# Optimization experiments

Measured on AMD Instinct MI355X. Metric: run time of the kernel, lower is better.

Reference implementation:

```python
import jax, jax.numpy as jnp
import numpy as np

DIM = 1024
NUM_HEADS = 16
HEAD_DIM = DIM // NUM_HEADS
SCALE = HEAD_DIM ** -0.5
B, N = 4, 2048


def setup_inputs() -> dict:
    key = jax.random.key(0)
    ks = jax.random.split(key, 5)
    s = 1.0 / np.sqrt(DIM)  # ~ torch Linear init scale
    x = jax.random.normal(ks[0], (B, N, DIM), dtype=jnp.float32)
    Wq = jax.random.normal(ks[1], (DIM, DIM), dtype=jnp.float32) * s
    Wk = jax.random.normal(ks[2], (DIM, DIM), dtype=jnp.float32) * s
    Wv = jax.random.normal(ks[3], (DIM, DIM), dtype=jnp.float32) * s
    Wo = jax.random.normal(ks[4], (DIM, DIM), dtype=jnp.float32) * s
    mask = jnp.tril(jnp.ones((N, N), dtype=bool))  # causal 2D bool mask
    return {"x": x, "mask": mask, "Wq": Wq, "Wk": Wk, "Wv": Wv, "Wo": Wo}


def reference(x, mask, Wq, Wk, Wv, Wo):
    Bb, Nn, D = x.shape
    def split_heads(t):
        return t.reshape(Bb, Nn, NUM_HEADS, HEAD_DIM).transpose(0, 2, 1, 3)  # [B,H,N,d]
    q = split_heads(x @ Wq.T)
    k = split_heads(x @ Wk.T)
    v = split_heads(x @ Wv.T)
    attn = jnp.einsum('bhqd,bhkd->bhqk', q, k) * SCALE  # [B,H,N,N]
    # 2D mask -> broadcast over batch and heads; ~mask positions set to -inf
    attn = jnp.where(mask[None, None, :, :], attn, -jnp.inf)
    attn = jax.nn.softmax(attn, axis=-1)
    out = jnp.einsum('bhqk,bhkd->bhqd', attn, v)
    out = out.transpose(0, 2, 1, 3).reshape(Bb, Nn, D)
    return out @ Wo.T
```

## Files before the change

### kernel.cpp

```cpp
#include <hip/hip_runtime.h>
#include <stdint.h>

#define Bq   4
#define Nseq 2048
#define NH   16
#define HD   64
#define DIMD 1024

typedef float  f32x4   __attribute__((ext_vector_type(4)));
typedef float  f32x16  __attribute__((ext_vector_type(16)));
typedef __bf16 bf16x8  __attribute__((ext_vector_type(8)));
typedef short  s16x4   __attribute__((ext_vector_type(4)));

typedef __attribute__((address_space(1))) void as1_void;
typedef __attribute__((address_space(3))) void as3_void;

static __device__ __forceinline__ uint16_t f2bf(float f) {
    uint32_t u = __builtin_bit_cast(uint32_t, f);
    u += 0x7fffu + ((u >> 16) & 1u);
    return (uint16_t)(u >> 16);
}

static __device__ __forceinline__ uint32_t pk2(float a, float b) {
    uint32_t ua = __builtin_bit_cast(uint32_t, a);
    uint32_t ub = __builtin_bit_cast(uint32_t, b);
    return (ua >> 16) | (ub & 0xffff0000u);
}

static __device__ __forceinline__ void asyncLoad16(const uint16_t* g, uint16_t* l) {
    __builtin_amdgcn_global_load_lds((as1_void*)g, (as3_void*)l, 16, 0, 0);
}

static __device__ __forceinline__ void storeOut(float* p, float v)    { *p = v; }
static __device__ __forceinline__ void storeOut(uint16_t* p, float v) { *p = f2bf(v); }

__global__ void cast_all(const float* __restrict__ x,
                         const float* __restrict__ wq, const float* __restrict__ wk,
                         const float* __restrict__ wv, const float* __restrict__ wo,
                         uint16_t* __restrict__ dst) {
    size_t i = ((size_t)blockIdx.x * blockDim.x + threadIdx.x) * 4;
    const float* src; size_t off; float scale = 1.0f;
    if (i < 8388608) { src = x; off = i; }
    else {
        size_t wI = i - 8388608;
        size_t wi = wI >> 20;
        off = wI & 1048575;
        src = (wi == 0) ? wq : (wi == 1) ? wk : (wi == 2) ? wv : wo;
        if (wi == 0) scale = 0.18033688011112042f;
    }
    float4 v = *(const float4*)(src + off);
    ushort4 o;
    o.x = f2bf(v.x * scale); o.y = f2bf(v.y * scale);
    o.z = f2bf(v.z * scale); o.w = f2bf(v.w * scale);
    *(ushort4*)(dst + i) = o;
}

__global__ __launch_bounds__(512, 2) void gemm_qkv384(
    const uint16_t* __restrict__ A, const uint16_t* __restrict__ W0,
    uint16_t* __restrict__ C0, uint16_t* __restrict__ vtb)
{
    __shared__ __align__(16) uint16_t Asm[2][2][4096];
    __shared__ __align__(16) uint16_t Bsm[2][2][12288];

    const int t = threadIdx.x, lane = t & 63, w = t >> 6;
    const int wm = w >> 2, wn = w & 3;
    const int ln = lane & 15, l4 = lane >> 4;

    const int m0 = blockIdx.x * 128;
    const int n0 = blockIdx.y * 384;

    const int srow = t >> 3;
    const int sg   = (t & 7) ^ (srow & 7);
    const uint16_t* aBase = A + (size_t)(m0 + (srow >> 5)*64 + (srow & 31))*DIMD + sg*8;
    const uint16_t* bBase[3];
    #pragma unroll
    for (int j = 0; j < 3; ++j) {
        int f = j*64 + srow;
        int wnf = f / 48, off = f % 48;
        bBase[j] = W0 + (size_t)(n0 + wnf*96 + off)*DIMD + sg*8;
    }

#define SA(mh_, buf_, kk_) asyncLoad16(aBase + (size_t)(mh_)*32*DIMD + (kk_), \
        &Asm[buf_][mh_][t*8])
#define SB(nh_, j_, buf_, kk_) asyncLoad16(bBase[j_] + (size_t)(nh_)*48*DIMD + (kk_), \
        &Bsm[buf_][nh_][(j_)*4096 + t*8])

    SA(0,0,0); SA(1,0,0);
    SB(0,0,0,0); SB(0,1,0,0); SB(0,2,0,0);
    SB(1,0,0,0); SB(1,1,0,0); SB(1,2,0,0);
    SA(0,1,64);
    SB(0,0,1,64); SB(0,1,1,64); SB(0,2,1,64);
    asm volatile("s_waitcnt vmcnt(4)" ::: "memory");
    __builtin_amdgcn_s_barrier();

    const int cs0 = ( l4      ^ (ln & 7)) * 8;
    const int cs1 = ((4 + l4) ^ (ln & 7)) * 8;
    const int awo = wm*2048 + ln*64;
    const int bwo = wn*3072 + ln*64;

    bf16x8 af[2][2], bf0[3][2], bf1[3][2];
    f32x4 acc[4][6] = {};

#define LDA(mh_, buf_)                                                         \
    _Pragma("unroll")                                                          \
    for (int mf = 0; mf < 2; ++mf) {                                           \
        af[mf][0] = *(const bf16x8*)(&Asm[buf_][mh_][awo + mf*1024 + cs0]);    \
        af[mf][1] = *(const bf16x8*)(&Asm[buf_][mh_][awo + mf*1024 + cs1]);    \
    }
#define LDB(nh_, buf_, BF)                                                     \
    _Pragma("unroll")                                                          \
    for (int nf = 0; nf < 3; ++nf) {                                           \
        BF[nf][0] = *(const bf16x8*)(&Bsm[buf_][nh_][bwo + nf*1024 + cs0]);    \
        BF[nf][1] = *(const bf16x8*)(&Bsm[buf_][nh_][bwo + nf*1024 + cs1]);    \
    }
#define MFMA12(mh_, nh_, BF)                                                   \
    _Pragma("unroll")                                                          \
    for (int mf = 0; mf < 2; ++mf)                                             \
        _Pragma("unroll")                                                      \
        for (int nf = 0; nf < 3; ++nf) {                                       \
            acc[(mh_)*2+mf][(nh_)*3+nf] = __builtin_amdgcn_mfma_f32_16x16x32_bf16( \
                af[mf][0], BF[nf][0], acc[(mh_)*2+mf][(nh_)*3+nf], 0,0,0);     \
            acc[(mh_)*2+mf][(nh_)*3+nf] = __builtin_amdgcn_mfma_f32_16x16x32_bf16( \
                af[mf][1], BF[nf][1], acc[(mh_)*2+mf][(nh_)*3+nf], 0,0,0);     \
        }
#define BARR()  __builtin_amdgcn_s_barrier()
#define SCB0()  __builtin_amdgcn_sched_barrier(0)
#define LGKM()  asm volatile("s_waitcnt lgkmcnt(0)" ::: "memory")
#define PRIO1() __builtin_amdgcn_s_setprio(1)
#define PRIO0() __builtin_amdgcn_s_setprio(0)

    #pragma unroll 1
    for (int i = 0; i < 8; ++i) {
        const int kk1 = i*128 + 64, kk2 = i*128 + 128, kk3 = i*128 + 192;
        const bool pf = (i < 7);

        LDA(0,0); LDB(0,0,bf0);
        SA(1,1,kk1); SB(1,0,1,kk1);
        BARR(); LGKM(); SCB0();
        PRIO1(); MFMA12(0,0,bf0); PRIO0();
        SCB0(); BARR();

        LDB(1,0,bf1);
        SB(1,1,1,kk1); SB(1,2,1,kk1);
        BARR(); LGKM(); SCB0();
        PRIO1(); MFMA12(0,1,bf1); PRIO0();
        SCB0(); BARR();

        LDA(1,0);
        if (pf) { SA(0,0,kk2); SB(0,0,0,kk2); }
        BARR(); LGKM(); SCB0();
        PRIO1(); MFMA12(1,0,bf0); PRIO0();
        SCB0(); BARR();

        if (pf) { SB(0,1,0,kk2); SB(0,2,0,kk2); }
        BARR(); SCB0();
        PRIO1(); MFMA12(1,1,bf1); PRIO0();
        SCB0();
        if (pf) { asm volatile("s_waitcnt vmcnt(4)" ::: "memory"); }
        else    { asm volatile("s_waitcnt vmcnt(0)" ::: "memory"); }
        BARR();

        LDA(0,1); LDB(0,1,bf0);
        if (pf) { SA(1,0,kk2); SB(1,0,0,kk2); }
        BARR(); LGKM(); SCB0();
        PRIO1(); MFMA12(0,0,bf0); PRIO0();
        SCB0(); BARR();

        LDB(1,1,bf1);
        if (pf) { SB(1,1,0,kk2); SB(1,2,0,kk2); }
        BARR(); LGKM(); SCB0();
        PRIO1(); MFMA12(0,1,bf1); PRIO0();
        SCB0(); BARR();

        LDA(1,1);
        if (pf) { SA(0,1,kk3); SB(0,0,1,kk3); }
        BARR(); LGKM(); SCB0();
        PRIO1(); MFMA12(1,0,bf0); PRIO0();
        SCB0(); BARR();

        if (pf) { SB(0,1,1,kk3); SB(0,2,1,kk3); }
        BARR(); SCB0();
        PRIO1(); MFMA12(1,1,bf1); PRIO0();
        SCB0();
        if (pf) { asm volatile("s_waitcnt vmcnt(4)" ::: "memory"); BARR(); }
    }

#undef SA
#undef SB
#undef LDA
#undef LDB
#undef MFMA12

    #pragma unroll
    for (int mh = 0; mh < 2; ++mh)
      #pragma unroll
      for (int mf = 0; mf < 2; ++mf)
        #pragma unroll
        for (int nh = 0; nh < 2; ++nh)
          #pragma unroll
          for (int nf = 0; nf < 3; ++nf) {
              const f32x4 a4 = acc[mh*2+mf][nh*3+nf];
              int rowg = m0 + wm*64 + mh*32 + mf*16 + l4*4;
              int colg = n0 + wn*96 + nh*48 + nf*16 + ln;
              if (colg < 2048) {
                  uint16_t* C = C0 + (size_t)(colg >> 10) * 8388608;
                  int col = colg & 1023;
                  #pragma unroll
                  for (int r = 0; r < 4; ++r)
                      C[(size_t)(rowg + r)*1024 + col] = f2bf(a4[r]);
              } else {
                  int dg = colg - 2048;
                  int bb = rowg >> 11, nn = rowg & 2047;
                  ushort4 o4;
                  o4.x = f2bf(a4[0]); o4.y = f2bf(a4[1]);
                  o4.z = f2bf(a4[2]); o4.w = f2bf(a4[3]);
                  *(ushort4*)(vtb + ((size_t)(bb*1024 + dg))*Nseq + nn) = o4;
              }
          }
}

template <typename OutT>
__global__ __launch_bounds__(256) void gemm_bt(
    const uint16_t* __restrict__ A, const uint16_t* __restrict__ W0,
    OutT* __restrict__ C0, int K, int Nld, int blocksPerSec,
    size_t wSecStride, size_t cSecStride, uint16_t* __restrict__ vtb, int vSec)
{
    __shared__ __align__(16) uint16_t As[128*64];
    __shared__ __align__(16) uint16_t Bs[128*64];

    const int t = threadIdx.x, lane = t & 63, w = t >> 6;
    const int wr = w >> 1, wc = w & 1;
    const int half = lane >> 5, ml = lane & 31;

    const int m0  = blockIdx.x * 128;
    const int sec = blockIdx.y / blocksPerSec;
    const int n0  = (blockIdx.y % blocksPerSec) * 128;
    const uint16_t* Wp = W0 + (size_t)sec * wSecStride;
    OutT* C = C0 + (size_t)sec * cSecStride;

    int srow[4], sg[4];
    #pragma unroll
    for (int i = 0; i < 4; ++i) {
        int s = t + 256*i;
        srow[i] = s >> 3;
        sg[i]   = (s & 7) ^ (srow[i] & 7);
    }

    int arow[2], brow[2];
    #pragma unroll
    for (int i = 0; i < 2; ++i) {
        arow[i] = wr*64 + i*32 + ml;
        brow[i] = wc*64 + i*32 + ml;
    }

    f32x16 acc[2][2] = {};

    for (int k0 = 0; k0 < K; k0 += 64) {
        __syncthreads();
        #pragma unroll
        for (int i = 0; i < 4; ++i) {
            asyncLoad16(A  + (size_t)(m0 + srow[i])*K + k0 + sg[i]*8,
                        As + (size_t)(w*64 + 256*i)*8);
            asyncLoad16(Wp + (size_t)(n0 + srow[i])*K + k0 + sg[i]*8,
                        Bs + (size_t)(w*64 + 256*i)*8);
        }
        __syncthreads();

        #pragma unroll
        for (int s = 0; s < 4; ++s) {
            const int chunk = s*2 + half;
            bf16x8 af[2], bfr[2];
            #pragma unroll
            for (int i = 0; i < 2; ++i) {
                int m = arow[i];
                af[i]  = *(const bf16x8*)(As + (size_t)(m*8 + (chunk ^ (m & 7)))*8);
                int n = brow[i];
                bfr[i] = *(const bf16x8*)(Bs + (size_t)(n*8 + (chunk ^ (n & 7)))*8);
            }
            #pragma unroll
            for (int mt = 0; mt < 2; ++mt)
                #pragma unroll
                for (int nt = 0; nt < 2; ++nt)
                    acc[mt][nt] = __builtin_amdgcn_mfma_f32_32x32x16_bf16(
                        af[mt], bfr[nt], acc[mt][nt], 0, 0, 0);
        }
    }

    if (vtb != nullptr && sec == vSec) {
        #pragma unroll
        for (int mt = 0; mt < 2; ++mt)
            #pragma unroll
            for (int nt = 0; nt < 2; ++nt) {
                int colg = n0 + wc*64 + nt*32 + ml;
                int hh = colg >> 6, dd = colg & 63;
                #pragma unroll
                for (int g = 0; g < 4; ++g) {
                    int rowg = m0 + wr*64 + mt*32 + 8*g + 4*half;
                    int bb = rowg >> 11, nn = rowg & 2047;
                    ushort4 o4;
                    o4.x = f2bf(acc[mt][nt][4*g + 0]);
                    o4.y = f2bf(acc[mt][nt][4*g + 1]);
                    o4.z = f2bf(acc[mt][nt][4*g + 2]);
                    o4.w = f2bf(acc[mt][nt][4*g + 3]);
                    *(ushort4*)(vtb + ((size_t)((bb*NH + hh)*HD + dd))*Nseq + nn) = o4;
                }
            }
    } else {
        #pragma unroll
        for (int mt = 0; mt < 2; ++mt)
            #pragma unroll
            for (int nt = 0; nt < 2; ++nt) {
                int col = n0 + wc*64 + nt*32 + ml;
                #pragma unroll
                for (int r = 0; r < 16; ++r) {
                    int row = m0 + wr*64 + mt*32 + (r & 3) + 8*(r >> 2) + 4*half;
                    storeOut(&C[(size_t)row * Nld + col], acc[mt][nt][r]);
                }
            }
    }
}

__global__ __launch_bounds__(256, 3) void attn(
    const uint16_t* __restrict__ Q, const uint16_t* __restrict__ K,
    const uint16_t* __restrict__ Vt, uint16_t* __restrict__ O)
{
    __shared__ __align__(16) uint16_t Kb[3][64*64];
    __shared__ __align__(16) uint16_t Vb[3][64*64];

    const int t = threadIdx.x, lane = t & 63, w = t >> 6;
    const int quad = lane >> 4, c = lane & 15;
    const int y = blockIdx.y;
    const int qi = (y < 4) ? (15 - y) : (y < 8) ? (y + 4) : (y < 12) ? (y - 4) : (15 - y);
    const int q0 = qi * 128;
    const int bh = blockIdx.x, b = bh >> 4, h = bh & 15;
    const size_t tokBase = (size_t)b * Nseq;
    const int hcol = h * HD;
    uint16_t* Qs = (uint16_t*)Kb;

    #define STAGE_KV(k0_, buf_)                                             \
        _Pragma("unroll")                                                    \
        for (int i = 0; i < 2; ++i) {                                        \
            int s = t + 256*i;                                               \
            int row = s >> 3, gg = (s & 7) ^ (row & 7);                      \
            asyncLoad16(K + (tokBase + (k0_) + row)*DIMD + hcol + gg*8,      \
                        Kb[buf_] + (size_t)(w*64 + 256*i)*8);                \
            asyncLoad16(Vt + ((size_t)bh*HD + row)*Nseq + (k0_) + gg*8,      \
                        Vb[buf_] + (size_t)(w*64 + 256*i)*8);                \
        }

    #pragma unroll
    for (int i = 0; i < 4; ++i) {
        int s = t + 256*i;
        int row = s >> 3, gg = (s & 7) ^ (row & 7);
        asyncLoad16(Q + (tokBase + q0 + row)*DIMD + hcol + gg*8,
                    Qs + (size_t)(w*64 + 256*i)*8);
    }
    __syncthreads();
    bf16x8 qf[2][2];
    #pragma unroll
    for (int qt = 0; qt < 2; ++qt)
        #pragma unroll
        for (int ks = 0; ks < 2; ++ks) {
            int row = w*32 + qt*16 + c;
            int pos = (ks*4 + quad) ^ (row & 7);
            qf[qt][ks] = *(const bf16x8*)(Qs + (size_t)(row*8 + pos)*8);
        }
    __syncthreads();

    const int wrow0 = q0 + w*32;
    const int end = 2*qi + 2;
    STAGE_KV(0, 0);
    STAGE_KV(64, 1);

    f32x4  o[2][4] = {};
    float  l_lane[2] = {0.f, 0.f};
    int b0 = 0, b1 = 1, b2 = 2;

    for (int kt = 0; kt < end; ++kt) {
        const int k0 = kt * 64;

        if (kt + 1 < end) { asm volatile("s_waitcnt vmcnt(4)\n\ts_barrier" ::: "memory"); }
        else              { asm volatile("s_waitcnt vmcnt(0)\n\ts_barrier" ::: "memory"); }

        if (kt + 2 < end) { STAGE_KV((kt+2)*64, b2); }

        if (k0 <= wrow0 + 31) {
            const uint16_t* Ks = Kb[b0];
            const uint16_t* Vs = Vb[b0];

            f32x4 sv[2][4] = {};
            __builtin_amdgcn_s_setprio(1);
            #pragma unroll
            for (int nt = 0; nt < 4; ++nt)
                #pragma unroll
                for (int ks = 0; ks < 2; ++ks) {
                    int row = nt*16 + c;
                    int pos = (ks*4 + quad) ^ (row & 7);
                    bf16x8 kf = *(const bf16x8*)(Ks + (size_t)(row*8 + pos)*8);
                    sv[0][nt] = __builtin_amdgcn_mfma_f32_16x16x32_bf16(kf, qf[0][ks], sv[0][nt], 0, 0, 0);
                    sv[1][nt] = __builtin_amdgcn_mfma_f32_16x16x32_bf16(kf, qf[1][ks], sv[1][nt], 0, 0, 0);
                }
            __builtin_amdgcn_s_setprio(0);

            if (k0 + 63 > wrow0) {
                #pragma unroll
                for (int qt = 0; qt < 2; ++qt)
                    #pragma unroll
                    for (int nt = 0; nt < 4; ++nt)
                        #pragma unroll
                        for (int r = 0; r < 4; ++r) {
                            int kvg = k0 + nt*16 + quad*4 + r;
                            int qg  = wrow0 + qt*16 + c;
                            if (kvg > qg) sv[qt][nt][r] = -340.0f;
                        }
            }

            s16x4 pb[2][4];
            #pragma unroll
            for (int qt = 0; qt < 2; ++qt)
                #pragma unroll
                for (int nt = 0; nt < 4; ++nt) {
                    float p0 = __builtin_amdgcn_exp2f(sv[qt][nt][0]);
                    float p1 = __builtin_amdgcn_exp2f(sv[qt][nt][1]);
                    float p2 = __builtin_amdgcn_exp2f(sv[qt][nt][2]);
                    float p3 = __builtin_amdgcn_exp2f(sv[qt][nt][3]);
                    l_lane[qt] += (p0 + p1) + (p2 + p3);
                    union { uint32_t u[2]; s16x4 v; } pu;
                    pu.u[0] = pk2(p0, p1);
                    pu.u[1] = pk2(p2, p3);
                    pb[qt][nt] = pu.v;
                }

            __builtin_amdgcn_s_setprio(1);
            #pragma unroll
            for (int s4 = 0; s4 < 4; ++s4)
                #pragma unroll
                for (int dt = 0; dt < 4; ++dt) {
                    int row = dt*16 + c;
                    int chunk = s4*2 + (quad >> 1);
                    int pos = chunk ^ (row & 7);
                    s16x4 vf = *(const s16x4*)(Vs + (size_t)(row*8 + pos)*8 + (quad & 1)*4);
                    o[0][dt] = __builtin_amdgcn_mfma_f32_16x16x16bf16_1k(vf, pb[0][s4], o[0][dt], 0, 0, 0);
                    o[1][dt] = __builtin_amdgcn_mfma_f32_16x16x16bf16_1k(vf, pb[1][s4], o[1][dt], 0, 0, 0);
                }
            __builtin_amdgcn_s_setprio(0);
        }

        int tmp = b0; b0 = b1; b1 = b2; b2 = tmp;
    }

    #pragma unroll
    for (int qt = 0; qt < 2; ++qt) {
        float l = l_lane[qt];
        l += __shfl_xor(l, 16);
        l += __shfl_xor(l, 32);
        float inv = 1.0f / l;
        int tok = (int)(q0 + w*32 + qt*16 + c);
        #pragma unroll
        for (int dt = 0; dt < 4; ++dt) {
            ushort4 o4;
            o4.x = f2bf(o[qt][dt][0] * inv);
            o4.y = f2bf(o[qt][dt][1] * inv);
            o4.z = f2bf(o[qt][dt][2] * inv);
            o4.w = f2bf(o[qt][dt][3] * inv);
            *(ushort4*)(O + (tokBase + tok)*DIMD + hcol + dt*16 + quad*4) = o4;
        }
    }
    #undef STAGE_KV
}

extern "C" void kernel_launch(void* const* d_in, const int* in_sizes, int n_in,
                              void* d_out, int out_size, void* d_ws, size_t ws_size,
                              hipStream_t stream) {
    const float* x  = (const float*)d_in[0];
    const float* Wq = (const float*)d_in[2];
    const float* Wk = (const float*)d_in[3];
    const float* Wv = (const float*)d_in[4];
    const float* Wo = (const float*)d_in[5];

    uint16_t* ws  = (uint16_t*)d_ws;
    uint16_t* xb  = ws;
    uint16_t* wqb = ws + 8388608;
    uint16_t* wob = wqb + 3*1048576;
    uint16_t* qb  = ws + 12582912;
    uint16_t* kb  = qb + 8388608;
    uint16_t* vtb = kb + 8388608;
    uint16_t* ab  = xb;

    cast_all<<<12288, 256, 0, stream>>>(x, Wq, Wk, Wv, Wo, ws);

    gemm_qkv384<<<dim3(64, 8), 512, 0, stream>>>(xb, wqb, qb, vtb);

    attn<<<dim3(64, 16), 256, 0, stream>>>(qb, kb, vtb, ab);

    gemm_bt<float><<<dim3(64, 8), 256, 0, stream>>>(
        ab, wob, (float*)d_out, DIMD, DIMD, 8, (size_t)0, (size_t)0, nullptr, -1);
}
```

Before: 247.7 us.

## Replace output projection GEMM with pipelined 256x128 double-buffered kernel

The generic gemm_bt used for the output projection is replaced by a dedicated gemm_out256 kernel modeled on the QKV kernel: 512 threads, 256x128 tiles, double-buffered async global-to-LDS loads with phased barriers, priority raising around MFMA blocks, and 16x16x32 MFMAs. It aims to hide load latency behind compute instead of the load-sync-compute loop. The grid shrinks to 256 blocks, which may underfill the 256 CUs with one wave of large blocks, and the store pattern writes fp32 with 16-wide column runs.

```diff
diff --git a/kernel.cpp b/kernel.cpp
--- a/kernel.cpp
+++ b/kernel.cpp
@@ -30,9 +30,6 @@
 static __device__ __forceinline__ void asyncLoad16(const uint16_t* g, uint16_t* l) {
     __builtin_amdgcn_global_load_lds((as1_void*)g, (as3_void*)l, 16, 0, 0);
 }
-
-static __device__ __forceinline__ void storeOut(float* p, float v)    { *p = v; }
-static __device__ __forceinline__ void storeOut(uint16_t* p, float v) { *p = f2bf(v); }
 
 __global__ void cast_all(const float* __restrict__ x,
                          const float* __restrict__ wq, const float* __restrict__ wk,
@@ -55,6 +52,12 @@
     *(ushort4*)(dst + i) = o;
 }
 
+#define BARR()  __builtin_amdgcn_s_barrier()
+#define SCB0()  __builtin_amdgcn_sched_barrier(0)
+#define LGKM()  asm volatile("s_waitcnt lgkmcnt(0)" ::: "memory")
+#define PRIO1() __builtin_amdgcn_s_setprio(1)
+#define PRIO0() __builtin_amdgcn_s_setprio(0)
+
 __global__ __launch_bounds__(512, 2) void gemm_qkv384(
     const uint16_t* __restrict__ A, const uint16_t* __restrict__ W0,
     uint16_t* __restrict__ C0, uint16_t* __restrict__ vtb)
@@ -91,7 +94,7 @@
     SA(0,1,64);
     SB(0,0,1,64); SB(0,1,1,64); SB(0,2,1,64);
     asm volatile("s_waitcnt vmcnt(4)" ::: "memory");
-    __builtin_amdgcn_s_barrier();
+    BARR();
 
     const int cs0 = ( l4      ^ (ln & 7)) * 8;
     const int cs1 = ((4 + l4) ^ (ln & 7)) * 8;
@@ -123,11 +126,6 @@
             acc[(mh_)*2+mf][(nh_)*3+nf] = __builtin_amdgcn_mfma_f32_16x16x32_bf16( \
                 af[mf][1], BF[nf][1], acc[(mh_)*2+mf][(nh_)*3+nf], 0,0,0);     \
         }
-#define BARR()  __builtin_amdgcn_s_barrier()
-#define SCB0()  __builtin_amdgcn_sched_barrier(0)
-#define LGKM()  asm volatile("s_waitcnt lgkmcnt(0)" ::: "memory")
-#define PRIO1() __builtin_amdgcn_s_setprio(1)
-#define PRIO0() __builtin_amdgcn_s_setprio(0)
 
     #pragma unroll 1
     for (int i = 0; i < 8; ++i) {
@@ -219,105 +217,136 @@
           }
 }
 
-template <typename OutT>
-__global__ __launch_bounds__(256) void gemm_bt(
+__global__ __launch_bounds__(512, 2) void gemm_out256(
     const uint16_t* __restrict__ A, const uint16_t* __restrict__ W0,
-    OutT* __restrict__ C0, int K, int Nld, int blocksPerSec,
-    size_t wSecStride, size_t cSecStride, uint16_t* __restrict__ vtb, int vSec)
+    float* __restrict__ C)
 {
-    __shared__ __align__(16) uint16_t As[128*64];
-    __shared__ __align__(16) uint16_t Bs[128*64];
+    __shared__ __align__(16) uint16_t Asm[2][2][8192];
+    __shared__ __align__(16) uint16_t Bsm[2][2][4096];
 
     const int t = threadIdx.x, lane = t & 63, w = t >> 6;
-    const int wr = w >> 1, wc = w & 1;
-    const int half = lane >> 5, ml = lane & 31;
-
-    const int m0  = blockIdx.x * 128;
-    const int sec = blockIdx.y / blocksPerSec;
-    const int n0  = (blockIdx.y % blocksPerSec) * 128;
-    const uint16_t* Wp = W0 + (size_t)sec * wSecStride;
-    OutT* C = C0 + (size_t)sec * cSecStride;
-
-    int srow[4], sg[4];
+    const int wm = w >> 2, wn = w & 3;
+    const int ln = lane & 15, l4 = lane >> 4;
+
+    const int m0 = blockIdx.x * 256;
+    const int n0 = blockIdx.y * 128;
+
+    const int srow = t >> 3;
+    const int sg   = (t & 7) ^ (srow & 7);
+    const uint16_t* aBase = A + (size_t)(m0 + srow)*DIMD + sg*8;
+    const uint16_t* bBase = W0 + (size_t)(n0 + (srow >> 4)*32 + (srow & 15))*DIMD + sg*8;
+
+#define SA(mh_, j_, buf_, kk_) asyncLoad16(aBase + (size_t)((j_)*128 + (mh_)*64)*DIMD + (kk_), \
+        &Asm[buf_][mh_][(j_)*4096 + t*8])
+#define SB(nh_, buf_, kk_) asyncLoad16(bBase + (size_t)(nh_)*16*DIMD + (kk_), \
+        &Bsm[buf_][nh_][t*8])
+
+    SB(0,0,0); SB(1,0,0);
+    SA(0,0,0,0); SA(0,1,0,0);
+    SA(1,0,0,0); SA(1,1,0,0);
+    SB(0,1,64); SB(1,1,64);
+    SA(0,0,1,64); SA(0,1,1,64);
+    asm volatile("s_waitcnt vmcnt(4)" ::: "memory");
+    BARR();
+
+    const int cs0 = ( l4      ^ (ln & 7)) * 8;
+    const int cs1 = ((4 + l4) ^ (ln & 7)) * 8;
+    const int awo = wm*4096 + ln*64;
+    const int bwo = wn*1024 + ln*64;
+
+    bf16x8 af[4][2], bfA[2], bfB[2];
+    f32x4 acc[8][2] = {};
+
+#define LDA(mh_, buf_)                                                         \
+    _Pragma("unroll")                                                          \
+    for (int mf = 0; mf < 4; ++mf) {                                           \
+        af[mf][0] = *(const bf16x8*)(&Asm[buf_][mh_][awo + mf*1024 + cs0]);    \
+        af[mf][1] = *(const bf16x8*)(&Asm[buf_][mh_][awo + mf*1024 + cs1]);    \
+    }
+#define LDB(nh_, buf_, BF)                                                     \
+    BF[0] = *(const bf16x8*)(&Bsm[buf_][nh_][bwo + cs0]);                      \
+    BF[1] = *(const bf16x8*)(&Bsm[buf_][nh_][bwo + cs1]);
+#define MFMA8(mh_, nh_, BF)                                                    \
+    _Pragma("unroll")                                                          \
+    for (int mf = 0; mf < 4; ++mf) {                                           \
+        acc[(mh_)*4+mf][nh_] = __builtin_amdgcn_mfma_f32_16x16x32_bf16(        \
+            af[mf][0], BF[0], acc[(mh_)*4+mf][nh_], 0,0,0);                    \
+        acc[(mh_)*4+mf][nh_] = __builtin_amdgcn_mfma_f32_16x16x32_bf16(        \
+            af[mf][1], BF[1], acc[(mh_)*4+mf][nh_], 0,0,0);                    \
+    }
+
+    #pragma unroll 1
+    for (int i = 0; i < 8; ++i) {
+        const int kk1 = i*128 + 64, kk2 = i*128 + 128, kk3 = i*128 + 192;
+        const bool pf2 = (i < 7);
+        const bool pf3 = (i < 7);
+
+        LDA(0,0); LDB(0,0,bfA);
+        SA(1,0,1,kk1); SA(1,1,1,kk1);
+        BARR(); LGKM(); SCB0();
+        PRIO1(); MFMA8(0,0,bfA); PRIO0();
+        SCB0(); BARR();
+
+        LDB(1,0,bfB);
+        BARR(); LGKM(); SCB0();
+        PRIO1(); MFMA8(0,1,bfB); PRIO0();
+        SCB0(); BARR();
+
+        LDA(1,0);
+        if (pf2) { SB(0,0,kk2); SB(1,0,kk2); SA(0,0,0,kk2); SA(0,1,0,kk2); }
+        BARR(); LGKM(); SCB0();
+        PRIO1(); MFMA8(1,0,bfA); PRIO0();
+        SCB0(); BARR();
+
+        BARR(); SCB0();
+        PRIO1(); MFMA8(1,1,bfB); PRIO0();
+        SCB0();
+        if (pf2) { asm volatile("s_waitcnt vmcnt(4)" ::: "memory"); }
+        else     { asm volatile("s_waitcnt vmcnt(0)" ::: "memory"); }
+        BARR();
+
+        LDA(0,1); LDB(0,1,bfA);
+        if (pf2) { SA(1,0,0,kk2); SA(1,1,0,kk2); }
+        BARR(); LGKM(); SCB0();
+        PRIO1(); MFMA8(0,0,bfA); PRIO0();
+        SCB0(); BARR();
+
+        LDB(1,1,bfB);
+        BARR(); LGKM(); SCB0();
+        PRIO1(); MFMA8(0,1,bfB); PRIO0();
+        SCB0(); BARR();
+
+        LDA(1,1);
+        if (pf3) { SB(0,1,kk3); SB(1,1,kk3); SA(0,0,1,kk3); SA(0,1,1,kk3); }
+        BARR(); LGKM(); SCB0();
+        PRIO1(); MFMA8(1,0,bfA); PRIO0();
+        SCB0(); BARR();
+
+        BARR(); SCB0();
+        PRIO1(); MFMA8(1,1,bfB); PRIO0();
+        SCB0();
+        if (pf3) { asm volatile("s_waitcnt vmcnt(4)" ::: "memory"); BARR(); }
+    }
+
+#undef SA
+#undef SB
+#undef LDA
+#undef LDB
+#undef MFMA8
+
     #pragma unroll
-    for (int i = 0; i < 4; ++i) {
-        int s = t + 256*i;
-        srow[i] = s >> 3;
-        sg[i]   = (s & 7) ^ (srow[i] & 7);
-    }
-
-    int arow[2], brow[2];
-    #pragma unroll
-    for (int i = 0; i < 2; ++i) {
-        arow[i] = wr*64 + i*32 + ml;
-        brow[i] = wc*64 + i*32 + ml;
-    }
-
-    f32x16 acc[2][2] = {};
-
-    for (int k0 = 0; k0 < K; k0 += 64) {
-        __syncthreads();
+    for (int mh = 0; mh < 2; ++mh)
+      #pragma unroll
+      for (int mf = 0; mf < 4; ++mf)
         #pragma unroll
-        for (int i = 0; i < 4; ++i) {
-            asyncLoad16(A  + (size_t)(m0 + srow[i])*K + k0 + sg[i]*8,
-                        As + (size_t)(w*64 + 256*i)*8);
-            asyncLoad16(Wp + (size_t)(n0 + srow[i])*K + k0 + sg[i]*8,
-                        Bs + (size_t)(w*64 + 256*i)*8);
+        for (int nh = 0; nh < 2; ++nh) {
+            const f32x4 a4 = acc[mh*4+mf][nh];
+            int rowg = m0 + wm*128 + mh*64 + mf*16 + l4*4;
+            int colg = n0 + wn*32 + nh*16 + ln;
+            #pragma unroll
+            for (int r = 0; r < 4; ++r)
+                C[(size_t)(rowg + r)*1024 + colg] = a4[r];
         }
-        __syncthreads();
-
-        #pragma unroll
-        for (int s = 0; s < 4; ++s) {
-            const int chunk = s*2 + half;
-            bf16x8 af[2], bfr[2];
-            #pragma unroll
-            for (int i = 0; i < 2; ++i) {
-                int m = arow[i];
-                af[i]  = *(const bf16x8*)(As + (size_t)(m*8 + (chunk ^ (m & 7)))*8);
-                int n = brow[i];
-                bfr[i] = *(const bf16x8*)(Bs + (size_t)(n*8 + (chunk ^ (n & 7)))*8);
-            }
-            #pragma unroll
-            for (int mt = 0; mt < 2; ++mt)
-                #pragma unroll
-                for (int nt = 0; nt < 2; ++nt)
-                    acc[mt][nt] = __builtin_amdgcn_mfma_f32_32x32x16_bf16(
-                        af[mt], bfr[nt], acc[mt][nt], 0, 0, 0);
-        }
-    }
-
-    if (vtb != nullptr && sec == vSec) {
-        #pragma unroll
-        for (int mt = 0; mt < 2; ++mt)
-            #pragma unroll
-            for (int nt = 0; nt < 2; ++nt) {
-                int colg = n0 + wc*64 + nt*32 + ml;
-                int hh = colg >> 6, dd = colg & 63;
-                #pragma unroll
-                for (int g = 0; g < 4; ++g) {
-                    int rowg = m0 + wr*64 + mt*32 + 8*g + 4*half;
-                    int bb = rowg >> 11, nn = rowg & 2047;
-                    ushort4 o4;
-                    o4.x = f2bf(acc[mt][nt][4*g + 0]);
-                    o4.y = f2bf(acc[mt][nt][4*g + 1]);
-                    o4.z = f2bf(acc[mt][nt][4*g + 2]);
-                    o4.w = f2bf(acc[mt][nt][4*g + 3]);
-                    *(ushort4*)(vtb + ((size_t)((bb*NH + hh)*HD + dd))*Nseq + nn) = o4;
-                }
-            }
-    } else {
-        #pragma unroll
-        for (int mt = 0; mt < 2; ++mt)
-            #pragma unroll
-            for (int nt = 0; nt < 2; ++nt) {
-                int col = n0 + wc*64 + nt*32 + ml;
-                #pragma unroll
-                for (int r = 0; r < 16; ++r) {
-                    int row = m0 + wr*64 + mt*32 + (r & 3) + 8*(r >> 2) + 4*half;
-                    storeOut(&C[(size_t)row * Nld + col], acc[mt][nt][r]);
-                }
-            }
-    }
 }
 
 __global__ __launch_bounds__(256, 3) void attn(
@@ -493,6 +522,5 @@
 
     attn<<<dim3(64, 16), 256, 0, stream>>>(qb, kb, vtb, ab);
 
-    gemm_bt<float><<<dim3(64, 8), 256, 0, stream>>>(
-        ab, wob, (float*)d_out, DIMD, DIMD, 8, (size_t)0, (size_t)0, nullptr, -1);
-}
+    gemm_out256<<<dim3(32, 8), 512, 0, stream>>>(ab, wob, (float*)d_out);
+}
```

Result: no change. 242.8 us (-2.0%).
